# Kernel tuning notes

Hardware: AMD Instinct MI355X
Metric: run time of the kernel (lower is better)

Reference implementation:

```python
import jax, jax.numpy as jnp
import numpy as np

H = 0.1   # RK4 step size
Y0 = 1.0  # setpoint constant in the ODE
UC = 1.0  # constant input term 'u' in the original source


def _fun(x, Fs, k1, k2, k3, k4, k5, k6):
    # x: (4,) state. Returns dx/dt per fun_full.
    return jnp.stack([
        x[2],
        x[3],
        k1 * x[2] + k2 * x[0] + 0.5 * k3 * k4 * x[1] ** 2 + k4 * Fs,
        k5 * x[3] - (x[0] - Y0) * k3 * k6 * x[1] + k6 * UC,
    ])


def _rk4_step(x, Fs, k1, k2, k3, k4, k5, k6):
    K1 = _fun(x, Fs, k1, k2, k3, k4, k5, k6)
    K2 = _fun(x + H / 2 * K1, Fs, k1, k2, k3, k4, k5, k6)
    K3 = _fun(x + H / 2 * K2, Fs, k1, k2, k3, k4, k5, k6)
    K4 = _fun(x + H * K3, Fs, k1, k2, k3, k4, k5, k6)
    return x + H / 6 * (K1 + 2 * K2 + 2 * K3 + K4)


def setup_inputs() -> dict:
    key = jax.random.key(0)
    T = 200000
    u = jax.random.normal(key, (T,), dtype=jnp.float32)
    return {
        "u": u,
        "k1": jnp.float32(-0.5),
        "k2": jnp.float32(-2.0),
        "k3": jnp.float32(0.3),
        "k4": jnp.float32(1.5),
        "k5": jnp.float32(-0.8),
        "k6": jnp.float32(0.7),
    }


def reference(u, k1, k2, k3, k4, k5, k6):
    x0 = jnp.zeros(4, dtype=u.dtype)

    def step(x, Fs):
        x_next = _rk4_step(x, Fs, k1, k2, k3, k4, k5, k6)
        return x_next, x_next

    _, ys = jax.lax.scan(step, x0, u)
    return ys  # [T, 4]
```

## Files before the change

### kernel.cpp

```cpp
#include <hip/hip_runtime.h>


typedef float v2f __attribute__((ext_vector_type(2)));
typedef float v4f __attribute__((ext_vector_type(4)));

__device__ unsigned int g_done_ctr = 0;

static __device__ __forceinline__ void rk4_step_pk(
    v2f& P, v2f& V, v2f CD, v2f CA, v2f CB, v2f CC,
    v2f H2v, v2f Hv, v2f H6v, v2f TWOv)
{
    v2f m, b, t, s, f1, f2, f3, f4, yP, yV, zP, zV, wP, wV;
    asm volatile(
        "v_pk_mul_f32 %[m], %[P], %[P] op_sel:[1,1] op_sel_hi:[0,1]\n\t"
        "v_pk_fma_f32 %[b], %[CC], %[m], %[CD]\n\t"
        "v_pk_fma_f32 %[b], %[CB], %[P], %[b]\n\t"
        "v_pk_fma_f32 %[f1], %[CA], %[V], %[b]\n\t"
        "v_pk_fma_f32 %[yP], %[H2], %[V], %[P]\n\t"
        "v_pk_fma_f32 %[yV], %[H2], %[f1], %[V]\n\t"
        "v_pk_mul_f32 %[m], %[yP], %[yP] op_sel:[1,1] op_sel_hi:[0,1]\n\t"
        "v_pk_fma_f32 %[b], %[CC], %[m], %[CD]\n\t"
        "v_pk_fma_f32 %[b], %[CB], %[yP], %[b]\n\t"
        "v_pk_fma_f32 %[f2], %[CA], %[yV], %[b]\n\t"
        "v_pk_fma_f32 %[zP], %[H2], %[yV], %[P]\n\t"
        "v_pk_fma_f32 %[zV], %[H2], %[f2], %[V]\n\t"
        "v_pk_mul_f32 %[m], %[zP], %[zP] op_sel:[1,1] op_sel_hi:[0,1]\n\t"
        "v_pk_fma_f32 %[b], %[CC], %[m], %[CD]\n\t"
        "v_pk_fma_f32 %[b], %[CB], %[zP], %[b]\n\t"
        "v_pk_fma_f32 %[f3], %[CA], %[zV], %[b]\n\t"
        "v_pk_fma_f32 %[wP], %[H], %[zV], %[P]\n\t"
        "v_pk_fma_f32 %[wV], %[H], %[f3], %[V]\n\t"
        "v_pk_mul_f32 %[m], %[wP], %[wP] op_sel:[1,1] op_sel_hi:[0,1]\n\t"
        "v_pk_fma_f32 %[b], %[CC], %[m], %[CD]\n\t"
        "v_pk_fma_f32 %[b], %[CB], %[wP], %[b]\n\t"
        "v_pk_fma_f32 %[f4], %[CA], %[wV], %[b]\n\t"
        "v_pk_fma_f32 %[t], %[TWO], %[yV], %[V]\n\t"
        "v_pk_fma_f32 %[t], %[TWO], %[zV], %[t]\n\t"
        "v_pk_add_f32 %[t], %[t], %[wV]\n\t"
        "v_pk_fma_f32 %[P], %[H6], %[t], %[P]\n\t"
        "v_pk_fma_f32 %[s], %[TWO], %[f2], %[f1]\n\t"
        "v_pk_fma_f32 %[s], %[TWO], %[f3], %[s]\n\t"
        "v_pk_add_f32 %[s], %[s], %[f4]\n\t"
        "v_pk_fma_f32 %[V], %[H6], %[s], %[V]\n\t"
        : [P]"+v"(P), [V]"+v"(V),
          [m]"=&v"(m), [b]"=&v"(b), [t]"=&v"(t), [s]"=&v"(s),
          [f1]"=&v"(f1), [f2]"=&v"(f2), [f3]"=&v"(f3), [f4]"=&v"(f4),
          [yP]"=&v"(yP), [yV]"=&v"(yV), [zP]"=&v"(zP), [zV]"=&v"(zV),
          [wP]"=&v"(wP), [wV]"=&v"(wV)
        : [CD]"v"(CD), [CA]"v"(CA), [CB]"v"(CB), [CC]"v"(CC),
          [H2]"v"(H2v), [H]"v"(Hv), [H6]"v"(H6v), [TWO]"v"(TWOv));
}

__global__ void cd_precompute_kernel(const float* __restrict__ u,
                                     const float* __restrict__ pk4,
                                     const float* __restrict__ pk6,
                                     v2f* __restrict__ cd, int T)
{
    const int t = blockIdx.x * 256 + threadIdx.x;
    if (t < T) {
        v2f c;
        c.x = (*pk4) * u[t];
        c.y = (*pk6) * 1.0f;
        cd[t] = c;
    }
}

#define DECL_SET(p) v2f p##0,p##1,p##2,p##3,p##4,p##5,p##6,p##7, \
                        p##8,p##9,p##10,p##11,p##12,p##13,p##14,p##15;
#define LOAD_SET(p, base) \
    p##0=(base)[0];  p##1=(base)[1];  p##2=(base)[2];  p##3=(base)[3];   \
    p##4=(base)[4];  p##5=(base)[5];  p##6=(base)[6];  p##7=(base)[7];   \
    p##8=(base)[8];  p##9=(base)[9];  p##10=(base)[10]; p##11=(base)[11];\
    p##12=(base)[12]; p##13=(base)[13]; p##14=(base)[14]; p##15=(base)[15];
#define DO_STEP(CDv, J)                                               \
    rk4_step_pk(P, V, CDv, CA, CB, CC, H2v, Hv, H6v, TWOv);           \
    ob[2*(J)]   = P;                                                  \
    ob[2*(J)+1] = V;
#define STEPS_SET(p)                                                  \
    DO_STEP(p##0,0)  DO_STEP(p##1,1)  DO_STEP(p##2,2)  DO_STEP(p##3,3)\
    DO_STEP(p##4,4)  DO_STEP(p##5,5)  DO_STEP(p##6,6)  DO_STEP(p##7,7)\
    DO_STEP(p##8,8)  DO_STEP(p##9,9)  DO_STEP(p##10,10) DO_STEP(p##11,11)\
    DO_STEP(p##12,12) DO_STEP(p##13,13) DO_STEP(p##14,14) DO_STEP(p##15,15)

__global__ void __launch_bounds__(256, 1)
rk4_chain_kernel(const float* __restrict__ u, const v2f* __restrict__ cdp,
                 const float* __restrict__ pk1, const float* __restrict__ pk2,
                 const float* __restrict__ pk3, const float* __restrict__ pk4,
                 const float* __restrict__ pk5, const float* __restrict__ pk6,
                 v2f* __restrict__ out2, int T)
{
    if (blockIdx.x != 0) {
        const unsigned v0 = atomicAdd(&g_done_ctr, 0u);
        float a0 = (float)threadIdx.x + 1.0f, a1 = a0 + 0.5f, a2 = a0 + 1.5f,
              a3 = a0 + 2.5f, a4 = a0 + 3.5f, a5 = a0 + 4.5f, a6 = a0 + 5.5f,
              a7 = a0 + 6.5f;
        const float mu = 1.0000001f, ad = 0.4999999f;
        for (long it = 0; it < 20000000L; ++it) {
            a0 = __builtin_fmaf(a0, mu, ad); a1 = __builtin_fmaf(a1, mu, ad);
            a2 = __builtin_fmaf(a2, mu, ad); a3 = __builtin_fmaf(a3, mu, ad);
            a4 = __builtin_fmaf(a4, mu, ad); a5 = __builtin_fmaf(a5, mu, ad);
            a6 = __builtin_fmaf(a6, mu, ad); a7 = __builtin_fmaf(a7, mu, ad);
            if ((it & 1023) == 0) {
                if (atomicAdd(&g_done_ctr, 0u) != v0) break;
            }
        }
        asm volatile("" :: "v"(a0), "v"(a1), "v"(a2), "v"(a3),
                           "v"(a4), "v"(a5), "v"(a6), "v"(a7));
        return;
    }
    if (threadIdx.x != 0) return;

    const float k1 = *pk1, k2 = *pk2, k3 = *pk3;
    const float k4 = *pk4, k5 = *pk5, k6 = *pk6;

    const float c034 = 0.5f * k3 * k4;
    const float k36  = k3 * k6;
    const float k6u  = k6 * 1.0f;

    const v2f CA   = { k1,    k5   };
    const v2f CB   = { k2,    k36  };
    const v2f CC   = { c034, -k36  };
    const v2f H2v  = { 0.05f, 0.05f };
    const v2f Hv   = { 0.1f,  0.1f  };
    const v2f H6v  = { 0.1f / 6.0f, 0.1f / 6.0f };
    const v2f TWOv = { 2.0f,  2.0f };

    v2f P = { 0.f, 0.f };
    v2f V = { 0.f, 0.f };

    v2f* ob = out2;
    const int nb = T >> 4;
    int b = 0;

    if (cdp != nullptr) {
        if (nb >= 1) {
            DECL_SET(A) DECL_SET(B)
            LOAD_SET(A, cdp)
            for (; b + 1 < nb; b += 2) {
                const v2f* nB = cdp + (size_t)(b + 1) * 16;
                LOAD_SET(B, nB)
                STEPS_SET(A)
                ob += 32;
                const v2f* nA = cdp + (size_t)((b + 2 < nb) ? b + 2 : nb - 1) * 16;
                LOAD_SET(A, nA)
                STEPS_SET(B)
                ob += 32;
            }
            if (b < nb) {
                STEPS_SET(A)
                ob += 32;
                ++b;
            }
        }
    } else {
        for (; b < nb; ++b) {
            const float* ub = u + (size_t)b * 16;
            DECL_SET(A)
            A0.x=k4*ub[0];  A0.y=k6u;  A1.x=k4*ub[1];  A1.y=k6u;
            A2.x=k4*ub[2];  A2.y=k6u;  A3.x=k4*ub[3];  A3.y=k6u;
            A4.x=k4*ub[4];  A4.y=k6u;  A5.x=k4*ub[5];  A5.y=k6u;
            A6.x=k4*ub[6];  A6.y=k6u;  A7.x=k4*ub[7];  A7.y=k6u;
            A8.x=k4*ub[8];  A8.y=k6u;  A9.x=k4*ub[9];  A9.y=k6u;
            A10.x=k4*ub[10]; A10.y=k6u; A11.x=k4*ub[11]; A11.y=k6u;
            A12.x=k4*ub[12]; A12.y=k6u; A13.x=k4*ub[13]; A13.y=k6u;
            A14.x=k4*ub[14]; A14.y=k6u; A15.x=k4*ub[15]; A15.y=k6u;
            STEPS_SET(A)
            ob += 32;
        }
    }

    for (int t = nb << 4; t < T; ++t) {
        v2f cdv; cdv.x = k4 * u[t]; cdv.y = k6u;
        rk4_step_pk(P, V, cdv, CA, CB, CC, H2v, Hv, H6v, TWOv);
        out2[2 * t]     = P;
        out2[2 * t + 1] = V;
    }

    __threadfence();
    atomicAdd(&g_done_ctr, 1u);
}

extern "C" void kernel_launch(void* const* d_in, const int* in_sizes, int n_in,
                              void* d_out, int out_size, void* d_ws, size_t ws_size,
                              hipStream_t stream)
{
    const float* u   = (const float*)d_in[0];
    const float* pk1 = (const float*)d_in[1];
    const float* pk2 = (const float*)d_in[2];
    const float* pk3 = (const float*)d_in[3];
    const float* pk4 = (const float*)d_in[4];
    const float* pk5 = (const float*)d_in[5];
    const float* pk6 = (const float*)d_in[6];
    v2f* out2 = (v2f*)d_out;
    const int T = in_sizes[0];

    v2f* cd = nullptr;
    if (ws_size >= (size_t)T * sizeof(v2f)) {
        cd = (v2f*)d_ws;
        const int pre_blocks = (T + 255) / 256;
        hipLaunchKernelGGL(cd_precompute_kernel, dim3(pre_blocks), dim3(256),
                           0, stream, u, pk4, pk6, cd, T);
    }

    hipLaunchKernelGGL(rk4_chain_kernel, dim3(256), dim3(256), 0, stream,
                       u, cd, pk1, pk2, pk3, pk4, pk5, pk6, out2, T);
}
```

Measured before the change: 14.79 ms.

## Algebraically restructure RK4 step to shorten dependency chain and precompute next-step terms

Rewrites the packed RK4 step so stage states are expressed through folded constants (H*H/6, k*H/2, etc.). This lets the position and velocity updates be computed in parallel FMA chains rather than sequential stage accumulations. It also computes the next step's first-stage bias and product term (a1, m1) at the end of the current step, pulling them off the critical path. The goal is a shorter serial latency per time step in this single-thread recurrence. In exchange, floating-point rounding changes and the macro plumbing becomes more intricate.

```diff
diff --git a/kernel.cpp b/kernel.cpp
--- a/kernel.cpp
+++ b/kernel.cpp
@@ -6,49 +6,46 @@
 
 __device__ unsigned int g_done_ctr = 0;
 
-static __device__ __forceinline__ void rk4_step_pk(
-    v2f& P, v2f& V, v2f CD, v2f CA, v2f CB, v2f CC,
-    v2f H2v, v2f Hv, v2f H6v, v2f TWOv)
-{
-    v2f m, b, t, s, f1, f2, f3, f4, yP, yV, zP, zV, wP, wV;
-    asm volatile(
-        "v_pk_mul_f32 %[m], %[P], %[P] op_sel:[1,1] op_sel_hi:[0,1]\n\t"
-        "v_pk_fma_f32 %[b], %[CC], %[m], %[CD]\n\t"
-        "v_pk_fma_f32 %[b], %[CB], %[P], %[b]\n\t"
-        "v_pk_fma_f32 %[f1], %[CA], %[V], %[b]\n\t"
-        "v_pk_fma_f32 %[yP], %[H2], %[V], %[P]\n\t"
-        "v_pk_fma_f32 %[yV], %[H2], %[f1], %[V]\n\t"
-        "v_pk_mul_f32 %[m], %[yP], %[yP] op_sel:[1,1] op_sel_hi:[0,1]\n\t"
-        "v_pk_fma_f32 %[b], %[CC], %[m], %[CD]\n\t"
-        "v_pk_fma_f32 %[b], %[CB], %[yP], %[b]\n\t"
-        "v_pk_fma_f32 %[f2], %[CA], %[yV], %[b]\n\t"
-        "v_pk_fma_f32 %[zP], %[H2], %[yV], %[P]\n\t"
-        "v_pk_fma_f32 %[zV], %[H2], %[f2], %[V]\n\t"
-        "v_pk_mul_f32 %[m], %[zP], %[zP] op_sel:[1,1] op_sel_hi:[0,1]\n\t"
-        "v_pk_fma_f32 %[b], %[CC], %[m], %[CD]\n\t"
-        "v_pk_fma_f32 %[b], %[CB], %[zP], %[b]\n\t"
-        "v_pk_fma_f32 %[f3], %[CA], %[zV], %[b]\n\t"
-        "v_pk_fma_f32 %[wP], %[H], %[zV], %[P]\n\t"
-        "v_pk_fma_f32 %[wV], %[H], %[f3], %[V]\n\t"
-        "v_pk_mul_f32 %[m], %[wP], %[wP] op_sel:[1,1] op_sel_hi:[0,1]\n\t"
-        "v_pk_fma_f32 %[b], %[CC], %[m], %[CD]\n\t"
-        "v_pk_fma_f32 %[b], %[CB], %[wP], %[b]\n\t"
-        "v_pk_fma_f32 %[f4], %[CA], %[wV], %[b]\n\t"
-        "v_pk_fma_f32 %[t], %[TWO], %[yV], %[V]\n\t"
-        "v_pk_fma_f32 %[t], %[TWO], %[zV], %[t]\n\t"
-        "v_pk_add_f32 %[t], %[t], %[wV]\n\t"
-        "v_pk_fma_f32 %[P], %[H6], %[t], %[P]\n\t"
-        "v_pk_fma_f32 %[s], %[TWO], %[f2], %[f1]\n\t"
-        "v_pk_fma_f32 %[s], %[TWO], %[f3], %[s]\n\t"
-        "v_pk_add_f32 %[s], %[s], %[f4]\n\t"
-        "v_pk_fma_f32 %[V], %[H6], %[s], %[V]\n\t"
-        : [P]"+v"(P), [V]"+v"(V),
-          [m]"=&v"(m), [b]"=&v"(b), [t]"=&v"(t), [s]"=&v"(s),
-          [f1]"=&v"(f1), [f2]"=&v"(f2), [f3]"=&v"(f3), [f4]"=&v"(f4),
-          [yP]"=&v"(yP), [yV]"=&v"(yV), [zP]"=&v"(zP), [zV]"=&v"(zV),
-          [wP]"=&v"(wP), [wV]"=&v"(wV)
-        : [CD]"v"(CD), [CA]"v"(CA), [CB]"v"(CB), [CC]"v"(CC),
-          [H2]"v"(H2v), [H]"v"(Hv), [H6]"v"(H6v), [TWO]"v"(TWOv));
+#define RK4_STEP(CDv, CDNv)                                                   \
+{                                                                             \
+    v2f r0, r1, r2, r3, r4, r5, r6, r7;                                       \
+    asm volatile(                                                             \
+        "v_pk_fma_f32 %[r0], %[H2c], %[V], %[P]\n\t"         \
+        "v_pk_fma_f32 %[r1], %[Hc],  %[V], %[P]\n\t"         \
+        "v_pk_fma_f32 %[r2], %[CAc], %[V], %[CD]\n\t"        \
+        "v_pk_fma_f32 %[r3], %[CAc], %[V], %[a1]\n\t"        \
+        "v_pk_mul_f32 %[r4], %[r0], %[r0] op_sel:[1,1] op_sel_hi:[0,1]\n\t"   \
+        "v_pk_fma_f32 %[r5], %[CBc], %[r0], %[r2]\n\t"       \
+        "v_pk_fma_f32 %[r6], %[CCc], %[m1], %[r3]\n\t"       \
+        "v_pk_fma_f32 %[r5], %[CCc], %[r4], %[r5]\n\t"       \
+        "v_pk_fma_f32 %[r3], %[H2q], %[r6], %[r0]\n\t"       \
+        "v_pk_fma_f32 %[r0], %[H6c], %[r6], %[V]\n\t"        \
+        "v_pk_fma_f32 %[r4], %[Hq6], %[r6], %[r1]\n\t"       \
+        "v_pk_fma_f32 %[r7], %[cH2], %[r6], %[r5]\n\t"       \
+        "v_pk_mul_f32 %[r5], %[r3], %[r3] op_sel:[1,1] op_sel_hi:[0,1]\n\t"   \
+        "v_pk_fma_f32 %[r6], %[CBc], %[r3], %[r2]\n\t"       \
+        "v_pk_fma_f32 %[r3], %[HH2], %[r7], %[r1]\n\t"       \
+        "v_pk_fma_f32 %[r1], %[H3c], %[r7], %[r0]\n\t"       \
+        "v_pk_fma_f32 %[r0], %[Hq6], %[r7], %[r4]\n\t"       \
+        "v_pk_fma_f32 %[r6], %[CCc], %[r5], %[r6]\n\t"       \
+        "v_pk_mul_f32 %[r5], %[r3], %[r3] op_sel:[1,1] op_sel_hi:[0,1]\n\t"   \
+        "v_pk_fma_f32 %[r4], %[CBc], %[r3], %[r2]\n\t"       \
+        "v_pk_fma_f32 %[r2], %[cH2], %[r7], %[r6]\n\t"       \
+        "v_pk_fma_f32 %[r4], %[CCc], %[r5], %[r4]\n\t"       \
+        "v_pk_fma_f32 %[r1], %[H3c], %[r2], %[r1]\n\t"       \
+        "v_pk_fma_f32 %[P],  %[Hq6], %[r2], %[r0]\n\t"       \
+        "v_pk_fma_f32 %[r0], %[cHc], %[r2], %[r4]\n\t"       \
+        "v_pk_mul_f32 %[m1], %[P], %[P] op_sel:[1,1] op_sel_hi:[0,1]\n\t"     \
+        "v_pk_fma_f32 %[a1], %[CBc], %[P], %[CDN]\n\t"       \
+        "v_pk_fma_f32 %[V],  %[H6c], %[r0], %[r1]\n\t"       \
+        : [P]"+v"(P), [V]"+v"(V), [a1]"+v"(a1), [m1]"+v"(m1),                 \
+          [r0]"=&v"(r0), [r1]"=&v"(r1), [r2]"=&v"(r2), [r3]"=&v"(r3),         \
+          [r4]"=&v"(r4), [r5]"=&v"(r5), [r6]"=&v"(r6), [r7]"=&v"(r7)          \
+        : [CD]"v"(CDv), [CDN]"v"(CDNv),                                       \
+          [CAc]"v"(CAc), [CBc]"v"(CBc), [CCc]"v"(CCc),                        \
+          [cH2]"v"(cH2), [cHc]"v"(cHc), [H2c]"v"(H2c), [Hc]"v"(Hc),           \
+          [H2q]"v"(H2q), [HH2]"v"(HH2), [H6c]"v"(H6c), [H3c]"v"(H3c),         \
+          [Hq6]"v"(Hq6));                                                     \
 }
 
 __global__ void cd_precompute_kernel(const float* __restrict__ u,
@@ -72,15 +69,17 @@
     p##4=(base)[4];  p##5=(base)[5];  p##6=(base)[6];  p##7=(base)[7];   \
     p##8=(base)[8];  p##9=(base)[9];  p##10=(base)[10]; p##11=(base)[11];\
     p##12=(base)[12]; p##13=(base)[13]; p##14=(base)[14]; p##15=(base)[15];
-#define DO_STEP(CDv, J)                                               \
-    rk4_step_pk(P, V, CDv, CA, CB, CC, H2v, Hv, H6v, TWOv);           \
+#define DO_STEP(CDv, CDNv, J)                                         \
+    RK4_STEP(CDv, CDNv)                                               \
     ob[2*(J)]   = P;                                                  \
     ob[2*(J)+1] = V;
-#define STEPS_SET(p)                                                  \
-    DO_STEP(p##0,0)  DO_STEP(p##1,1)  DO_STEP(p##2,2)  DO_STEP(p##3,3)\
-    DO_STEP(p##4,4)  DO_STEP(p##5,5)  DO_STEP(p##6,6)  DO_STEP(p##7,7)\
-    DO_STEP(p##8,8)  DO_STEP(p##9,9)  DO_STEP(p##10,10) DO_STEP(p##11,11)\
-    DO_STEP(p##12,12) DO_STEP(p##13,13) DO_STEP(p##14,14) DO_STEP(p##15,15)
+#define STEPS_SET(p, NX)                                                     \
+    DO_STEP(p##0,p##1,0)   DO_STEP(p##1,p##2,1)   DO_STEP(p##2,p##3,2)       \
+    DO_STEP(p##3,p##4,3)   DO_STEP(p##4,p##5,4)   DO_STEP(p##5,p##6,5)       \
+    DO_STEP(p##6,p##7,6)   DO_STEP(p##7,p##8,7)   DO_STEP(p##8,p##9,8)       \
+    DO_STEP(p##9,p##10,9)  DO_STEP(p##10,p##11,10) DO_STEP(p##11,p##12,11)   \
+    DO_STEP(p##12,p##13,12) DO_STEP(p##13,p##14,13) DO_STEP(p##14,p##15,14)  \
+    DO_STEP(p##15, NX, 15)
 
 __global__ void __launch_bounds__(256, 1)
 rk4_chain_kernel(const float* __restrict__ u, const v2f* __restrict__ cdp,
@@ -91,20 +90,20 @@
 {
     if (blockIdx.x != 0) {
         const unsigned v0 = atomicAdd(&g_done_ctr, 0u);
-        float a0 = (float)threadIdx.x + 1.0f, a1 = a0 + 0.5f, a2 = a0 + 1.5f,
+        float a0 = (float)threadIdx.x + 1.0f, a1s = a0 + 0.5f, a2s = a0 + 1.5f,
               a3 = a0 + 2.5f, a4 = a0 + 3.5f, a5 = a0 + 4.5f, a6 = a0 + 5.5f,
               a7 = a0 + 6.5f;
         const float mu = 1.0000001f, ad = 0.4999999f;
         for (long it = 0; it < 20000000L; ++it) {
-            a0 = __builtin_fmaf(a0, mu, ad); a1 = __builtin_fmaf(a1, mu, ad);
-            a2 = __builtin_fmaf(a2, mu, ad); a3 = __builtin_fmaf(a3, mu, ad);
+            a0 = __builtin_fmaf(a0, mu, ad); a1s = __builtin_fmaf(a1s, mu, ad);
+            a2s = __builtin_fmaf(a2s, mu, ad); a3 = __builtin_fmaf(a3, mu, ad);
             a4 = __builtin_fmaf(a4, mu, ad); a5 = __builtin_fmaf(a5, mu, ad);
             a6 = __builtin_fmaf(a6, mu, ad); a7 = __builtin_fmaf(a7, mu, ad);
             if ((it & 1023) == 0) {
                 if (atomicAdd(&g_done_ctr, 0u) != v0) break;
             }
         }
-        asm volatile("" :: "v"(a0), "v"(a1), "v"(a2), "v"(a3),
+        asm volatile("" :: "v"(a0), "v"(a1s), "v"(a2s), "v"(a3),
                            "v"(a4), "v"(a5), "v"(a6), "v"(a7));
         return;
     }
@@ -116,14 +115,23 @@
     const float c034 = 0.5f * k3 * k4;
     const float k36  = k3 * k6;
     const float k6u  = k6 * 1.0f;
-
-    const v2f CA   = { k1,    k5   };
-    const v2f CB   = { k2,    k36  };
-    const v2f CC   = { c034, -k36  };
-    const v2f H2v  = { 0.05f, 0.05f };
-    const v2f Hv   = { 0.1f,  0.1f  };
-    const v2f H6v  = { 0.1f / 6.0f, 0.1f / 6.0f };
-    const v2f TWOv = { 2.0f,  2.0f };
+    const float H2   = 0.05f;
+    const float Hf   = 0.1f;
+    const float H6   = 0.1f / 6.0f;
+    const float H3   = 0.1f / 3.0f;
+
+    const v2f CAc = { k1,        k5        };
+    const v2f CBc = { k2,        k36       };
+    const v2f CCc = { c034,     -k36       };
+    const v2f cH2 = { k1 * H2,   k5 * H2   };
+    const v2f cHc = { k1 * Hf,   k5 * Hf   };
+    const v2f H2c = { H2,        H2        };
+    const v2f Hc  = { Hf,        Hf        };
+    const v2f H2q = { H2 * H2,   H2 * H2   };
+    const v2f HH2 = { Hf * H2,   Hf * H2   };
+    const v2f H6c = { H6,        H6        };
+    const v2f H3c = { H3,        H3        };
+    const v2f Hq6 = { Hf * Hf / 6.0f, Hf * Hf / 6.0f };
 
     v2f P = { 0.f, 0.f };
     v2f V = { 0.f, 0.f };
@@ -136,23 +144,30 @@
         if (nb >= 1) {
             DECL_SET(A) DECL_SET(B)
             LOAD_SET(A, cdp)
+            v2f a1, m1;
+            a1.x = __builtin_fmaf(k2,  P.x, A0.x);
+            a1.y = __builtin_fmaf(k36, P.y, A0.y);
+            m1.x = P.y * P.y;
+            m1.y = P.x * P.y;
             for (; b + 1 < nb; b += 2) {
                 const v2f* nB = cdp + (size_t)(b + 1) * 16;
                 LOAD_SET(B, nB)
-                STEPS_SET(A)
+                STEPS_SET(A, B0)
                 ob += 32;
                 const v2f* nA = cdp + (size_t)((b + 2 < nb) ? b + 2 : nb - 1) * 16;
                 LOAD_SET(A, nA)
-                STEPS_SET(B)
+                STEPS_SET(B, A0)
                 ob += 32;
             }
             if (b < nb) {
-                STEPS_SET(A)
+                STEPS_SET(A, A15)
                 ob += 32;
                 ++b;
             }
         }
     } else {
+        v2f a1, m1;
+        bool init = false;
         for (; b < nb; ++b) {
             const float* ub = u + (size_t)b * 16;
             DECL_SET(A)
@@ -164,14 +179,29 @@
             A10.x=k4*ub[10]; A10.y=k6u; A11.x=k4*ub[11]; A11.y=k6u;
             A12.x=k4*ub[12]; A12.y=k6u; A13.x=k4*ub[13]; A13.y=k6u;
             A14.x=k4*ub[14]; A14.y=k6u; A15.x=k4*ub[15]; A15.y=k6u;
-            STEPS_SET(A)
+            if (!init) {
+                a1.x = __builtin_fmaf(k2,  P.x, A0.x);
+                a1.y = __builtin_fmaf(k36, P.y, A0.y);
+                m1.x = P.y * P.y;
+                m1.y = P.x * P.y;
+                init = true;
+            }
+            v2f NX;
+            if (b + 1 < nb) { NX.x = k4 * ub[16]; NX.y = k6u; }
+            else            { NX = A15; }
+            STEPS_SET(A, NX)
             ob += 32;
         }
     }
 
     for (int t = nb << 4; t < T; ++t) {
         v2f cdv; cdv.x = k4 * u[t]; cdv.y = k6u;
-        rk4_step_pk(P, V, cdv, CA, CB, CC, H2v, Hv, H6v, TWOv);
+        v2f a1, m1;
+        a1.x = __builtin_fmaf(k2,  P.x, cdv.x);
+        a1.y = __builtin_fmaf(k36, P.y, cdv.y);
+        m1.x = P.y * P.y;
+        m1.y = P.x * P.y;
+        RK4_STEP(cdv, cdv)
         out2[2 * t]     = P;
         out2[2 * t + 1] = V;
     }
```

Measured after the change: 12.51 ms. 1.18x faster.
